# Kernel tuning notes

Hardware: AMD Instinct MI355X
Metric: run time of the kernel (lower is better)

Reference implementation:

```python
import jax, jax.numpy as jnp
import numpy as np

B, M, IN, OUT = 4096, 8, 512, 512


def setup_inputs() -> dict:
    key = jax.random.key(0)
    k1, k2 = jax.random.split(key)
    x = jax.random.normal(k1, (B, M, IN), dtype=jnp.float32)
    # xavier_uniform over (n_mode, in, out): fan_in=IN, fan_out=OUT
    limit = float(np.sqrt(6.0 / (IN + OUT)))
    weight = jax.random.uniform(k2, (M, IN, OUT), dtype=jnp.float32,
                                minval=-limit, maxval=limit)
    bias = jnp.zeros((M, OUT), dtype=jnp.float32)
    return {"input": x, "weight": weight, "bias": bias}


def reference(input, weight, bias):
    # torch: (weight * input.unsqueeze(-1)).sum(-2) + bias
    # == per-mode linear: out[b,m,o] = sum_i input[b,m,i] * weight[m,i,o] + bias[m,o]
    out = jnp.einsum('bmi,mio->bmo', input, weight)
    return out + bias
```

## Files before the change

kernel.cpp:

```cpp
#include <hip/hip_runtime.h>
#include <hip/hip_bf16.h>


#define B_   4096
#define M_   8
#define IN_  512
#define OUT_ 512
#define BM   128
#define BN   128
#define BK   32

typedef __attribute__((ext_vector_type(8))) short  short8;
typedef __attribute__((ext_vector_type(4))) float  f32x4;
typedef __attribute__((ext_vector_type(4))) int    i32x4;

static __device__ inline unsigned f2bf2(float lo, float hi) {
  union { float f; unsigned u; } a, b;
  a.f = lo; b.f = hi;
  unsigned ua = a.u + 0x7FFFu + ((a.u >> 16) & 1u);
  unsigned ub = b.u + 0x7FFFu + ((b.u >> 16) & 1u);
  return (ua >> 16) | (ub & 0xFFFF0000u);
}

static __device__ inline i32x4 pack8(f32x4 u, f32x4 v) {
  i32x4 r;
  r[0] = f2bf2(u[0], u[1]);
  r[1] = f2bf2(u[2], u[3]);
  r[2] = f2bf2(v[0], v[1]);
  r[3] = f2bf2(v[2], v[3]);
  return r;
}

extern "C" __global__ __launch_bounds__(256, 2)
void mmlin_kernel(const float* __restrict__ X, const float* __restrict__ W,
                  const float* __restrict__ Bias, float* __restrict__ O) {
  __shared__ unsigned char lds[16384];

  const int t    = threadIdx.x;
  const int lane = t & 63;
  const int w    = t >> 6;

  const int b0 = blockIdx.x * BM;
  const int n0 = blockIdx.y * BN;
  const int m  = blockIdx.z;

  const int ar  = t >> 1;
  const int ac0 = (t & 1) * 16;
  const float* aptr = X + (size_t)(b0 + ar) * (M_ * IN_) + m * IN_ + ac0;
  const int swzA  = (ar & 7) << 4;
  const int a_st0 = (ar * 64 + ac0 * 2)      ^ swzA;
  const int a_st1 = (ar * 64 + ac0 * 2 + 16) ^ swzA;

  const int bc  = t & 127;
  const int bk0 = (t >> 7) * 16;
  const float* bptr = W + (size_t)m * IN_ * OUT_ + (size_t)bk0 * OUT_ + n0 + bc;
  const int swzB  = (bc & 7) << 4;
  const int b_st0 = (8192 + bc * 64 + bk0 * 2)      ^ swzB;
  const int b_st1 = (8192 + bc * 64 + bk0 * 2 + 16) ^ swzB;

  const int wr  = (w >> 1) * 64;
  const int wc  = (w & 1)  * 64;
  const int fr  = lane & 15;
  const int fkB = (lane >> 4) * 16;

  int a_ld[4], b_ld[4];
#pragma unroll
  for (int mi = 0; mi < 4; ++mi) {
    int row = wr + mi * 16 + fr;
    a_ld[mi] = (row * 64 + fkB) ^ ((row & 7) << 4);
  }
#pragma unroll
  for (int ni = 0; ni < 4; ++ni) {
    int col = wc + ni * 16 + fr;
    b_ld[ni] = (8192 + col * 64 + fkB) ^ ((col & 7) << 4);
  }

  f32x4 acc[4][4] = {};

  f32x4 a_raw[4];
  float b_raw[16];
  {
    const f32x4* ap = (const f32x4*)aptr;
#pragma unroll
    for (int i = 0; i < 4; ++i) a_raw[i] = ap[i];
#pragma unroll
    for (int j = 0; j < 16; ++j) b_raw[j] = bptr[(size_t)j * OUT_];
  }
  i32x4 apk0 = pack8(a_raw[0], a_raw[1]);
  i32x4 apk1 = pack8(a_raw[2], a_raw[3]);
  i32x4 bpk0, bpk1;
  bpk0[0] = f2bf2(b_raw[0],  b_raw[1]);  bpk0[1] = f2bf2(b_raw[2],  b_raw[3]);
  bpk0[2] = f2bf2(b_raw[4],  b_raw[5]);  bpk0[3] = f2bf2(b_raw[6],  b_raw[7]);
  bpk1[0] = f2bf2(b_raw[8],  b_raw[9]);  bpk1[1] = f2bf2(b_raw[10], b_raw[11]);
  bpk1[2] = f2bf2(b_raw[12], b_raw[13]); bpk1[3] = f2bf2(b_raw[14], b_raw[15]);

  for (int kk = 0; kk < IN_; kk += BK) {
    __syncthreads();
    *(i32x4*)(lds + a_st0) = apk0;
    *(i32x4*)(lds + a_st1) = apk1;
    *(i32x4*)(lds + b_st0) = bpk0;
    *(i32x4*)(lds + b_st1) = bpk1;
    __syncthreads();

    const int kn = kk + BK;
    if (kn < IN_) {
      const f32x4* ap = (const f32x4*)(aptr + kn);
#pragma unroll
      for (int i = 0; i < 4; ++i) a_raw[i] = ap[i];
#pragma unroll
      for (int j = 0; j < 16; ++j) b_raw[j] = bptr[(size_t)(kn + j) * OUT_];
    }

    short8 af[4], bf4[4];
#pragma unroll
    for (int mi = 0; mi < 4; ++mi) af[mi]  = *(const short8*)(lds + a_ld[mi]);
#pragma unroll
    for (int ni = 0; ni < 4; ++ni) bf4[ni] = *(const short8*)(lds + b_ld[ni]);

#pragma unroll
    for (int mi = 0; mi < 4; ++mi)
#pragma unroll
      for (int ni = 0; ni < 4; ++ni)
        acc[mi][ni] = __builtin_amdgcn_mfma_f32_16x16x32_bf16(
            af[mi], bf4[ni], acc[mi][ni], 0, 0, 0);

    if (kn < IN_) {
      apk0 = pack8(a_raw[0], a_raw[1]);
      apk1 = pack8(a_raw[2], a_raw[3]);
      bpk0[0] = f2bf2(b_raw[0],  b_raw[1]);  bpk0[1] = f2bf2(b_raw[2],  b_raw[3]);
      bpk0[2] = f2bf2(b_raw[4],  b_raw[5]);  bpk0[3] = f2bf2(b_raw[6],  b_raw[7]);
      bpk1[0] = f2bf2(b_raw[8],  b_raw[9]);  bpk1[1] = f2bf2(b_raw[10], b_raw[11]);
      bpk1[2] = f2bf2(b_raw[12], b_raw[13]); bpk1[3] = f2bf2(b_raw[14], b_raw[15]);
    }
  }

#pragma unroll
  for (int ni = 0; ni < 4; ++ni) {
    const int col = n0 + wc + ni * 16 + fr;
    const float bs = Bias[m * OUT_ + col];
#pragma unroll
    for (int mi = 0; mi < 4; ++mi) {
#pragma unroll
      for (int r = 0; r < 4; ++r) {
        const int row = b0 + wr + mi * 16 + (lane >> 4) * 4 + r;
        O[(size_t)row * (M_ * OUT_) + m * OUT_ + col] = acc[mi][ni][r] + bs;
      }
    }
  }
}

extern "C" void kernel_launch(void* const* d_in, const int* in_sizes, int n_in,
                              void* d_out, int out_size, void* d_ws, size_t ws_size,
                              hipStream_t stream) {
  const float* X    = (const float*)d_in[0];
  const float* W    = (const float*)d_in[1];
  const float* Bias = (const float*)d_in[2];
  float* O = (float*)d_out;

  dim3 grid(B_ / BM, OUT_ / BN, M_);
  mmlin_kernel<<<grid, dim3(256), 0, stream>>>(X, W, Bias, O);
}
```

Measured before the change: 158.4 us.

## Pre-pack weights to bf16 and double-buffer async global-to-LDS loads

A prep kernel converts each weight tile to bf16 in the swizzled LDS layout and writes it to the workspace, so the main kernel no longer issues strided per-column float loads and converts W again in every block. The main kernel uses global_load_lds to copy X (still fp32) and the packed W straight into double-buffered LDS, and converts X to bf16 after reading it back from LDS. This overlaps the next tile's loads with the current tile's MFMAs and drops the register staging. In exchange it uses more LDS per block (48 KB), adds a second kernel launch each call, and falls back to the old kernel when the workspace is too small.

```diff
diff --git a/kernel.cpp b/kernel.cpp
--- a/kernel.cpp
+++ b/kernel.cpp
@@ -9,10 +9,15 @@
 #define BM   128
 #define BN   128
 #define BK   32
+#define NKT  (IN_ / BK)
+#define WS_NEED (M_ * 4 * 16 * 8192)
 
 typedef __attribute__((ext_vector_type(8))) short  short8;
 typedef __attribute__((ext_vector_type(4))) float  f32x4;
 typedef __attribute__((ext_vector_type(4))) int    i32x4;
+
+#define GLB(p) ((const __attribute__((address_space(1))) void*)(p))
+#define LDS(p) ((__attribute__((address_space(3))) void*)(p))
 
 static __device__ inline unsigned f2bf2(float lo, float hi) {
   union { float f; unsigned u; } a, b;
@@ -22,24 +27,162 @@
   return (ua >> 16) | (ub & 0xFFFF0000u);
 }
 
-static __device__ inline i32x4 pack8(f32x4 u, f32x4 v) {
-  i32x4 r;
-  r[0] = f2bf2(u[0], u[1]);
-  r[1] = f2bf2(u[2], u[3]);
-  r[2] = f2bf2(v[0], v[1]);
-  r[3] = f2bf2(v[2], v[3]);
-  return r;
-}
+union pk8 { i32x4 i; short8 s; };
 
 extern "C" __global__ __launch_bounds__(256, 2)
-void mmlin_kernel(const float* __restrict__ X, const float* __restrict__ W,
-                  const float* __restrict__ Bias, float* __restrict__ O) {
+void prep_w(const float* __restrict__ W, unsigned char* __restrict__ ws) {
+  const int c  = blockIdx.x;
+  const int kb = c & 15;
+  const int nbm = c >> 4;
+  const int nb = nbm & 3;
+  const int m  = nbm >> 2;
+
+  __shared__ float tile[32][132];
+
+  const int t  = threadIdx.x;
+  {
+    const int k  = t >> 3;
+    const int n4 = (t & 7) * 16;
+    const float* src = W + (size_t)m * (IN_ * OUT_) + (size_t)(kb * 32 + k) * OUT_ + nb * 128 + n4;
+#pragma unroll
+    for (int i = 0; i < 4; ++i) {
+      f32x4 v = *(const f32x4*)(src + i * 4);
+      tile[k][n4 + i * 4 + 0] = v[0];
+      tile[k][n4 + i * 4 + 1] = v[1];
+      tile[k][n4 + i * 4 + 2] = v[2];
+      tile[k][n4 + i * 4 + 3] = v[3];
+    }
+  }
+  __syncthreads();
+
+  unsigned char* out = ws + (size_t)c * 8192;
+#pragma unroll
+  for (int s = t; s < 512; s += 256) {
+    const int col = s >> 2;
+    const int k8  = s & 3;
+    float f[8];
+#pragma unroll
+    for (int j = 0; j < 8; ++j) f[j] = tile[k8 * 8 + j][col];
+    i32x4 p;
+    p[0] = f2bf2(f[0], f[1]); p[1] = f2bf2(f[2], f[3]);
+    p[2] = f2bf2(f[4], f[5]); p[3] = f2bf2(f[6], f[7]);
+    const int phys = (col * 64 + k8 * 16) ^ ((col & 7) << 4);
+    *(i32x4*)(out + phys) = p;
+  }
+}
+
+extern "C" __global__ __launch_bounds__(256, 3)
+void mmlin_main(const float* __restrict__ X, const unsigned char* __restrict__ Wp,
+                const float* __restrict__ Bias, float* __restrict__ O) {
+  __shared__ unsigned char lds[49152];
+
+  const int t = threadIdx.x, l = t & 63, w = t >> 6;
+  const int b0 = blockIdx.x * BM;
+  const int nb = blockIdx.y;
+  const int n0 = nb * BN;
+  const int m  = blockIdx.z;
+
+  const char* Xb = (const char*)X;
+  const char* a_src[4];
+  int a_dst[4];
+#pragma unroll
+  for (int i = 0; i < 4; ++i) {
+    const int j = w * 4 + i;
+    a_src[i] = Xb + (size_t)(b0 + j * 8 + (l >> 3)) * (M_ * IN_ * 4)
+             + m * (IN_ * 4)
+             + (((l & 7) ^ (l >> 3)) << 4);
+    a_dst[i] = j * 1024 + l * 16;
+  }
+  const unsigned char* b_src = Wp + (size_t)((m * 4 + nb) * 16) * 8192 + (w * 2) * 1024 + l * 16;
+  const int b_dst = 32768 + (w * 2) * 1024 + l * 16;
+
+  const int wr = (w >> 1) * 64, wc = (w & 1) * 64;
+  const int fr = l & 15, g = l >> 4;
+  int aoff0[4], aoff1[4], boff[4];
+#pragma unroll
+  for (int mi = 0; mi < 4; ++mi) {
+    const int row = wr + mi * 16 + fr;
+    aoff0[mi] = row * 128 + (((2 * g)     ^ (row & 7)) << 4);
+    aoff1[mi] = row * 128 + (((2 * g + 1) ^ (row & 7)) << 4);
+  }
+#pragma unroll
+  for (int ni = 0; ni < 4; ++ni) {
+    const int col = wc + ni * 16 + fr;
+    boff[ni] = 32768 + ((col * 64 + g * 16) ^ ((col & 7) << 4));
+  }
+
+  f32x4 acc[4][4] = {};
+
+#pragma unroll
+  for (int i = 0; i < 4; ++i)
+    __builtin_amdgcn_global_load_lds(GLB(a_src[i]), LDS(lds + a_dst[i]), 16, 0, 0);
+#pragma unroll
+  for (int i = 0; i < 2; ++i)
+    __builtin_amdgcn_global_load_lds(GLB(b_src + i * 1024), LDS(lds + b_dst + i * 1024), 16, 0, 0);
+
+  for (int kt = 0; kt < NKT; ++kt) {
+    __syncthreads();
+    const int cur = kt & 1;
+    const int nxt = cur ^ 1;
+
+    if (kt + 1 < NKT) {
+#pragma unroll
+      for (int i = 0; i < 4; ++i)
+        __builtin_amdgcn_global_load_lds(GLB(a_src[i] + (kt + 1) * (BK * 4)),
+                                         LDS(lds + nxt * 16384 + a_dst[i]), 16, 0, 0);
+#pragma unroll
+      for (int i = 0; i < 2; ++i)
+        __builtin_amdgcn_global_load_lds(GLB(b_src + (size_t)(kt + 1) * 8192 + i * 1024),
+                                         LDS(lds + nxt * 8192 + b_dst + i * 1024), 16, 0, 0);
+    }
+
+    const unsigned char* A  = lds + cur * 16384;
+    const unsigned char* Bb = lds + cur * 8192;
+
+    short8 af[4], bf[4];
+#pragma unroll
+    for (int mi = 0; mi < 4; ++mi) {
+      f32x4 q0 = *(const f32x4*)(A + aoff0[mi]);
+      f32x4 q1 = *(const f32x4*)(A + aoff1[mi]);
+      pk8 p;
+      p.i[0] = f2bf2(q0[0], q0[1]); p.i[1] = f2bf2(q0[2], q0[3]);
+      p.i[2] = f2bf2(q1[0], q1[1]); p.i[3] = f2bf2(q1[2], q1[3]);
+      af[mi] = p.s;
+    }
+#pragma unroll
+    for (int ni = 0; ni < 4; ++ni)
+      bf[ni] = *(const short8*)(Bb + boff[ni]);
+
+#pragma unroll
+    for (int mi = 0; mi < 4; ++mi)
+#pragma unroll
+      for (int ni = 0; ni < 4; ++ni)
+        acc[mi][ni] = __builtin_amdgcn_mfma_f32_16x16x32_bf16(
+            af[mi], bf[ni], acc[mi][ni], 0, 0, 0);
+  }
+
+#pragma unroll
+  for (int ni = 0; ni < 4; ++ni) {
+    const int col = n0 + wc + ni * 16 + fr;
+    const float bs = Bias[m * OUT_ + col];
+#pragma unroll
+    for (int mi = 0; mi < 4; ++mi) {
+#pragma unroll
+      for (int r = 0; r < 4; ++r) {
+        const int row = b0 + wr + mi * 16 + g * 4 + r;
+        O[(size_t)row * (M_ * OUT_) + m * OUT_ + col] = acc[mi][ni][r] + bs;
+      }
+    }
+  }
+}
+
+extern "C" __global__ __launch_bounds__(256, 2)
+void mmlin_fallback(const float* __restrict__ X, const float* __restrict__ W,
+                    const float* __restrict__ Bias, float* __restrict__ O) {
   __shared__ unsigned char lds[16384];
-
-  const int t    = threadIdx.x;
+  const int t = threadIdx.x;
   const int lane = t & 63;
-  const int w    = t >> 6;
-
+  const int w = t >> 6;
   const int b0 = blockIdx.x * BM;
   const int n0 = blockIdx.y * BN;
   const int m  = blockIdx.z;
@@ -58,9 +201,8 @@
   const int b_st0 = (8192 + bc * 64 + bk0 * 2)      ^ swzB;
   const int b_st1 = (8192 + bc * 64 + bk0 * 2 + 16) ^ swzB;
 
-  const int wr  = (w >> 1) * 64;
-  const int wc  = (w & 1)  * 64;
-  const int fr  = lane & 15;
+  const int wr = (w >> 1) * 64, wc = (w & 1) * 64;
+  const int fr = lane & 15;
   const int fkB = (lane >> 4) * 16;
 
   int a_ld[4], b_ld[4];
@@ -76,7 +218,6 @@
   }
 
   f32x4 acc[4][4] = {};
-
   f32x4 a_raw[4];
   float b_raw[16];
   {
@@ -86,9 +227,11 @@
 #pragma unroll
     for (int j = 0; j < 16; ++j) b_raw[j] = bptr[(size_t)j * OUT_];
   }
-  i32x4 apk0 = pack8(a_raw[0], a_raw[1]);
-  i32x4 apk1 = pack8(a_raw[2], a_raw[3]);
-  i32x4 bpk0, bpk1;
+  i32x4 apk0, apk1, bpk0, bpk1;
+  apk0[0] = f2bf2(a_raw[0][0], a_raw[0][1]); apk0[1] = f2bf2(a_raw[0][2], a_raw[0][3]);
+  apk0[2] = f2bf2(a_raw[1][0], a_raw[1][1]); apk0[3] = f2bf2(a_raw[1][2], a_raw[1][3]);
+  apk1[0] = f2bf2(a_raw[2][0], a_raw[2][1]); apk1[1] = f2bf2(a_raw[2][2], a_raw[2][3]);
+  apk1[2] = f2bf2(a_raw[3][0], a_raw[3][1]); apk1[3] = f2bf2(a_raw[3][2], a_raw[3][3]);
   bpk0[0] = f2bf2(b_raw[0],  b_raw[1]);  bpk0[1] = f2bf2(b_raw[2],  b_raw[3]);
   bpk0[2] = f2bf2(b_raw[4],  b_raw[5]);  bpk0[3] = f2bf2(b_raw[6],  b_raw[7]);
   bpk1[0] = f2bf2(b_raw[8],  b_raw[9]);  bpk1[1] = f2bf2(b_raw[10], b_raw[11]);
@@ -125,8 +268,10 @@
             af[mi], bf4[ni], acc[mi][ni], 0, 0, 0);
 
     if (kn < IN_) {
-      apk0 = pack8(a_raw[0], a_raw[1]);
-      apk1 = pack8(a_raw[2], a_raw[3]);
+      apk0[0] = f2bf2(a_raw[0][0], a_raw[0][1]); apk0[1] = f2bf2(a_raw[0][2], a_raw[0][3]);
+      apk0[2] = f2bf2(a_raw[1][0], a_raw[1][1]); apk0[3] = f2bf2(a_raw[1][2], a_raw[1][3]);
+      apk1[0] = f2bf2(a_raw[2][0], a_raw[2][1]); apk1[1] = f2bf2(a_raw[2][2], a_raw[2][3]);
+      apk1[2] = f2bf2(a_raw[3][0], a_raw[3][1]); apk1[3] = f2bf2(a_raw[3][2], a_raw[3][3]);
       bpk0[0] = f2bf2(b_raw[0],  b_raw[1]);  bpk0[1] = f2bf2(b_raw[2],  b_raw[3]);
       bpk0[2] = f2bf2(b_raw[4],  b_raw[5]);  bpk0[3] = f2bf2(b_raw[6],  b_raw[7]);
       bpk1[0] = f2bf2(b_raw[8],  b_raw[9]);  bpk1[1] = f2bf2(b_raw[10], b_raw[11]);
@@ -158,5 +303,10 @@
   float* O = (float*)d_out;
 
   dim3 grid(B_ / BM, OUT_ / BN, M_);
-  mmlin_kernel<<<grid, dim3(256), 0, stream>>>(X, W, Bias, O);
-}
+  if (ws_size >= (size_t)WS_NEED) {
+    prep_w<<<dim3(512), dim3(256), 0, stream>>>(W, (unsigned char*)d_ws);
+    mmlin_main<<<grid, dim3(256), 0, stream>>>(X, (const unsigned char*)d_ws, Bias, O);
+  } else {
+    mmlin_fallback<<<grid, dim3(256), 0, stream>>>(X, W, Bias, O);
+  }
+}
```

After: 153.2 us. 3.3% less time.
